# Optimization experiments

Hardware: AMD Instinct MI355X
Metric: run time of the kernel (lower is better)

The kernel has to match this reference:

```python
import jax, jax.numpy as jnp
import numpy as np

N_LEVELS = 12
BASE_RES = 16
PER_LEVEL_SCALE = 2.0
TABLE_SIZE = 1 << 20  # 2**log2_hashmap_size
PRIME_Y = np.uint32(2654435761)
FIRST_OMEGA = 300.0
HIDDEN_OMEGA = 1.0


def hash_grid_encode(table, coords):
    """tcnn-style multi-resolution hash grid, linear interpolation.
    table: [L, T, F] float32, coords: [N, 2] in [0, 1). Returns [N, L*F]."""
    feats = []
    for lvl in range(N_LEVELS):
        res = int(np.floor(BASE_RES * (PER_LEVEL_SCALE ** lvl)))
        pos = coords * res                       # [N, 2]
        i0 = jnp.floor(pos)
        w = pos - i0                             # fractional part, [N, 2]
        i0 = i0.astype(jnp.int32)
        dense = (res + 1) ** 2 <= TABLE_SIZE     # static per level
        acc = 0.0
        for dx, dy in ((0, 0), (1, 0), (0, 1), (1, 1)):
            ix = i0[:, 0] + dx
            iy = i0[:, 1] + dy
            if dense:
                idx = ix + iy * (res + 1)
            else:
                h = ix.astype(jnp.uint32) ^ (iy.astype(jnp.uint32) * PRIME_Y)
                idx = (h & jnp.uint32(TABLE_SIZE - 1)).astype(jnp.int32)
            wx = w[:, 0] if dx else (1.0 - w[:, 0])
            wy = w[:, 1] if dy else (1.0 - w[:, 1])
            acc = acc + table[lvl, idx] * (wx * wy)[:, None]
        feats.append(acc)
    return jnp.concatenate(feats, axis=-1)       # [N, 24]


def setup_inputs() -> dict:
    key = jax.random.key(0)
    ks = jax.random.split(key, 12)
    N = 1 << 20
    coords = jax.random.uniform(ks[0], (N, 2), dtype=jnp.float32)
    # tcnn default grid init: uniform(-1e-4, 1e-4)
    table = jax.random.uniform(ks[1], (N_LEVELS, TABLE_SIZE, 2), dtype=jnp.float32,
                               minval=-1e-4, maxval=1e-4)
    # first layer: normal(0, 0.1) per first_init_type='normal'
    W0 = 0.1 * jax.random.normal(ks[2], (24, 16), dtype=jnp.float32)
    b0 = jax.random.uniform(ks[3], (16,), dtype=jnp.float32,
                            minval=-1 / np.sqrt(24), maxval=1 / np.sqrt(24))
    # siren init for hidden/final: uniform(+-sqrt(6/fan_in)/omega), omega=1
    bnd = np.sqrt(6.0 / 16.0)
    W1 = jax.random.uniform(ks[4], (16, 16), jnp.float32, -bnd, bnd)
    b1 = jax.random.uniform(ks[5], (16,), jnp.float32, -0.25, 0.25)
    W2 = jax.random.uniform(ks[6], (16, 16), jnp.float32, -bnd, bnd)
    b2 = jax.random.uniform(ks[7], (16,), jnp.float32, -0.25, 0.25)
    W3 = jax.random.uniform(ks[8], (16, 1), jnp.float32, -bnd, bnd)
    b3 = jax.random.uniform(ks[9], (1,), jnp.float32, -0.25, 0.25)
    return {"coords": coords, "table": table, "W0": W0, "b0": b0,
            "W1": W1, "b1": b1, "W2": W2, "b2": b2, "W3": W3, "b3": b3}


def reference(coords, table, W0, b0, W1, b1, W2, b2, W3, b3):
    enc = hash_grid_encode(table, coords)               # [N, 24]
    h = jnp.sin(FIRST_OMEGA * (enc @ W0 + b0))          # SineLayer, omega_0=300
    h = jnp.sin(HIDDEN_OMEGA * (h @ W1 + b1))
    h = jnp.sin(HIDDEN_OMEGA * (h @ W2 + b2))
    return h @ W3 + b3                                  # outermost linear, [N, 1]
```

## Files before the change

### kernel.cpp

```cpp
#include <hip/hip_runtime.h>
#include <math.h>

#define TSIZE (1u << 20)
#define PRIME_Y 2654435761u
#define NHASH 6

typedef __attribute__((ext_vector_type(8))) short short8;
typedef __attribute__((ext_vector_type(4))) float f32x4;
typedef __attribute__((ext_vector_type(4))) float float4v;
typedef __attribute__((ext_vector_type(2))) float float2v;
typedef __attribute__((ext_vector_type(4))) unsigned uint4v;
typedef __attribute__((ext_vector_type(2))) unsigned uint2v;

struct alignas(8) f4a8 { float x, y, z, w; };

__device__ __forceinline__ unsigned bf16rne(unsigned u) {
    return (u + 0x7fffu + ((u >> 16) & 1u)) >> 16;
}
__device__ __forceinline__ unsigned pack_bf16x2(float a, float b) {
    return (bf16rne(__float_as_uint(a)) & 0xffffu) | (bf16rne(__float_as_uint(b)) << 16);
}
__device__ __forceinline__ float2 unpack_bf16x2(unsigned u) {
    float2 r;
    r.x = __uint_as_float(u << 16);
    r.y = __uint_as_float(u & 0xffff0000u);
    return r;
}
__device__ __forceinline__ short f2bf(float x) {
    return (short)(bf16rne(__float_as_uint(x)) & 0xffffu);
}
__device__ __forceinline__ float bf2f(short h) {
    return __uint_as_float(((unsigned)(unsigned short)h) << 16);
}
__device__ __forceinline__ unsigned hilo_pack(float v) {
    const unsigned uv = __float_as_uint(v);
    const float l = v - __uint_as_float(uv & 0xffff0000u);
    return (uv >> 16) | (__float_as_uint(l) & 0xffff0000u);
}

__device__ __forceinline__ unsigned fp8e(float f) {
    const float v = f * 8192.0f;
    const unsigned a = __float_as_uint(v);
    const unsigned sign = (a >> 31) << 7;
    const unsigned mag = a & 0x7fffffffu;
    const unsigned r = mag + 0x7ffffu + ((mag >> 20) & 1u);
    int u = (int)(r >> 20) - (120 << 3);
    u = (u < 0) ? 0 : u;
    return (unsigned)u | sign;
}
__device__ __forceinline__ float fp8d(unsigned u8) {
    const unsigned bits = ((u8 & 0x80u) << 24) |
                          (((u8 & 0x7fu) << 20) + (107u << 23));
    return __uint_as_float(bits);
}
__device__ __forceinline__ float2 fp8d2(unsigned u16) {
    float2 r;
    r.x = fp8d(u16 & 0xffu);
    r.y = fp8d((u16 >> 8) & 0xffu);
    return r;
}

__global__ __launch_bounds__(256) void convert_kernel(
    const float* __restrict__ table, unsigned* __restrict__ wtab8,
    const float* __restrict__ W0, const float* __restrict__ b0,
    const float* __restrict__ W1, const float* __restrict__ b1,
    const float* __restrict__ W2, const float* __restrict__ b2,
    const float* __restrict__ W3,
    uint4v* __restrict__ wfrag)
{
    if (blockIdx.x == 0 && threadIdx.x < 64) {
        const int lane = threadIdx.x;
        const int n = lane & 15;
        const int kb = lane >> 4;
        short8 bf0, b1a, b1b, b2a, b2b;
        #pragma unroll
        for (int j = 0; j < 8; ++j) {
            const int k = kb * 8 + j;
            bf0[j] = (k < 24) ? f2bf(W0[k * 16 + n]) : (short)0;
            const int i = k >> 1;
            const float w1 = W1[i * 16 + n];
            const float w2 = W2[i * 16 + n];
            const short w1h = f2bf(w1), w2h = f2bf(w2);
            b1a[j] = w1h;
            b2a[j] = w2h;
            b1b[j] = (k & 1) ? (short)0 : f2bf(w1 - bf2f(w1h));
            b2b[j] = (k & 1) ? (short)0 : f2bf(w2 - bf2f(w2h));
        }
        union { short8 s; uint4v u; } cv;
        cv.s = bf0; wfrag[0 * 64 + lane] = cv.u;
        cv.s = b1a; wfrag[1 * 64 + lane] = cv.u;
        cv.s = b1b; wfrag[2 * 64 + lane] = cv.u;
        cv.s = b2a; wfrag[3 * 64 + lane] = cv.u;
        cv.s = b2b; wfrag[4 * 64 + lane] = cv.u;
        float4v bb;
        bb.x = b0[n]; bb.y = b1[n]; bb.z = b2[n]; bb.w = W3[n];
        union { float4v f; uint4v u; } cf; cf.f = bb;
        wfrag[5 * 64 + lane] = cf.u;
    }
    const size_t total4 = (size_t)NHASH * TSIZE / 2;
    const float4v* __restrict__ src =
        reinterpret_cast<const float4v*>(table + (size_t)6 * TSIZE * 2);
    for (size_t i = (size_t)blockIdx.x * 256 + threadIdx.x; i < total4;
         i += (size_t)gridDim.x * 256) {
        float4v v = __builtin_nontemporal_load(&src[i]);
        wtab8[i] = fp8e(v.x) | (fp8e(v.y) << 8) | (fp8e(v.z) << 16) | (fp8e(v.w) << 24);
    }
}

__global__ __launch_bounds__(256) void pass_all_kernel(
    const float* __restrict__ coords,
    const unsigned* __restrict__ wtab8,
    unsigned* __restrict__ wenc,
    int bpl, int N)
{
    const int lvl = blockIdx.x / bpl;
    const int gid = (blockIdx.x - lvl * bpl) * 256 + threadIdx.x;
    const int base = gid * 4;
    if (base >= N) return;
    const int res = 16 << (lvl + 6);
    const unsigned* __restrict__ tlp = wtab8 + ((size_t)lvl * TSIZE >> 1);
    const unsigned short* __restrict__ tl8 =
        reinterpret_cast<const unsigned short*>(tlp);
    unsigned* __restrict__ we = wenc + (size_t)lvl * N;

    if (base + 3 < N) {
        const float4v* __restrict__ c4 = reinterpret_cast<const float4v*>(coords);
        const float4v ca = __builtin_nontemporal_load(&c4[gid * 2]);
        const float4v cb = __builtin_nontemporal_load(&c4[gid * 2 + 1]);
        const float xs[4] = {ca.x, ca.z, cb.x, cb.z};
        const float ys[4] = {ca.y, ca.w, cb.y, cb.w};
        unsigned h00a[4], h01a[4], h10a[4], h11a[4], oddp[4];
        float wxs[4], wys[4];
        #pragma unroll
        for (int p = 0; p < 4; ++p) {
            const float px = xs[p] * (float)res;
            const float py = ys[p] * (float)res;
            const float fx = floorf(px), fy = floorf(py);
            wxs[p] = px - fx;
            wys[p] = py - fy;
            const unsigned ux = (unsigned)(int)fx, uy = (unsigned)(int)fy;
            const unsigned hy0 = uy * PRIME_Y;
            const unsigned hy1 = (uy + 1u) * PRIME_Y;
            h00a[p] = (ux ^ hy0) & (TSIZE - 1u);
            h01a[p] = (ux ^ hy1) & (TSIZE - 1u);
            h10a[p] = ((ux + 1u) ^ hy0) & (TSIZE - 1u);
            h11a[p] = ((ux + 1u) ^ hy1) & (TSIZE - 1u);
            oddp[p] = ux & 1u;
        }
        unsigned pr0[4], pr1[4];
        #pragma unroll
        for (int p = 0; p < 4; ++p) {
            pr0[p] = tlp[h00a[p] >> 1];
            pr1[p] = tlp[h01a[p] >> 1];
        }
        unsigned t10[4], t11[4];
        #pragma unroll
        for (int p = 0; p < 4; ++p) { t10[p] = 0u; t11[p] = 0u; }
        #pragma unroll
        for (int p = 0; p < 4; ++p) {
            if (oddp[p]) {
                t10[p] = tl8[h10a[p]];
                t11[p] = tl8[h11a[p]];
            }
        }
        uint4v r;
        #pragma unroll
        for (int p = 0; p < 4; ++p) {
            const unsigned s0 = h00a[p] & 1u;
            const unsigned s1 = h01a[p] & 1u;
            const unsigned e00 = s0 ? (pr0[p] >> 16) : (pr0[p] & 0xffffu);
            const unsigned e01 = s1 ? (pr1[p] >> 16) : (pr1[p] & 0xffffu);
            const unsigned e10 = oddp[p] ? t10[p]
                                         : (s0 ? (pr0[p] & 0xffffu) : (pr0[p] >> 16));
            const unsigned e11 = oddp[p] ? t11[p]
                                         : (s1 ? (pr1[p] & 0xffffu) : (pr1[p] >> 16));
            const float wx = wxs[p], wy = wys[p];
            const float w00 = (1.0f - wx) * (1.0f - wy);
            const float w10 = wx * (1.0f - wy);
            const float w01 = (1.0f - wx) * wy;
            const float w11 = wx * wy;
            const float2 f00 = fp8d2(e00);
            const float2 f10 = fp8d2(e10);
            const float2 f01 = fp8d2(e01);
            const float2 f11 = fp8d2(e11);
            const float e0 = f00.x * w00 + f10.x * w10 + f01.x * w01 + f11.x * w11;
            const float e1 = f00.y * w00 + f10.y * w10 + f01.y * w01 + f11.y * w11;
            r[p] = pack_bf16x2(e0, e1);
        }
        ((uint4v*)we)[gid] = r;
    } else {
        for (int p = 0; p < 4 && base + p < N; ++p) {
            const float2 c = reinterpret_cast<const float2*>(coords)[base + p];
            const float px = c.x * (float)res;
            const float py = c.y * (float)res;
            const float fx = floorf(px), fy = floorf(py);
            const float wx = px - fx, wy = py - fy;
            const unsigned ux = (unsigned)(int)fx, uy = (unsigned)(int)fy;
            const unsigned hy0 = uy * PRIME_Y;
            const unsigned hy1 = (uy + 1u) * PRIME_Y;
            const float2 v00 = fp8d2(tl8[(ux ^ hy0) & (TSIZE - 1u)]);
            const float2 v10 = fp8d2(tl8[((ux + 1u) ^ hy0) & (TSIZE - 1u)]);
            const float2 v01 = fp8d2(tl8[(ux ^ hy1) & (TSIZE - 1u)]);
            const float2 v11 = fp8d2(tl8[((ux + 1u) ^ hy1) & (TSIZE - 1u)]);
            const float w00 = (1.0f - wx) * (1.0f - wy);
            const float w10 = wx * (1.0f - wy);
            const float w01 = (1.0f - wx) * wy;
            const float w11 = wx * wy;
            const float e0 = v00.x * w00 + v10.x * w10 + v01.x * w01 + v11.x * w11;
            const float e1 = v00.y * w00 + v10.y * w10 + v01.y * w01 + v11.y * w11;
            we[base + p] = pack_bf16x2(e0, e1);
        }
    }
}

__device__ __forceinline__ void stage_row(char* ldsw, int lane, const unsigned* u) {
    uint4v* rowp = (uint4v*)(ldsw + lane * 80);
    uint4v r0; r0.x = u[0]; r0.y = u[1]; r0.z = u[2]; r0.w = u[3];
    uint4v r1; r1.x = u[4]; r1.y = u[5]; r1.z = u[6]; r1.w = u[7];
    uint4v r2; r2.x = u[8]; r2.y = u[9]; r2.z = u[10]; r2.w = u[11];
    uint4v r3; r3.x = 0u; r3.y = 0u; r3.z = 0u; r3.w = 0u;
    rowp[0] = r0; rowp[1] = r1; rowp[2] = r2; rowp[3] = r3;
}

__global__ __launch_bounds__(256) void mlp_kernel(
    const float* __restrict__ coords,
    const float* __restrict__ table,
    const unsigned* __restrict__ wenc,
    const uint4v* __restrict__ wfrag,
    const float* __restrict__ b3p,
    float* __restrict__ out, int N)
{
    __shared__ char lds[40960];
    const int t = threadIdx.x;
    const int lane = t & 63;
    const int wv = t >> 6;
    const int n = lane & 15;
    const int kb = lane >> 4;
    char* lds0 = lds + wv * 10240;
    char* lds1 = lds0 + 5120;

    union { short8 s; uint4v u; } w0u, w1au, w1bu, w2au, w2bu;
    w0u.u  = wfrag[0 * 64 + lane];
    w1au.u = wfrag[1 * 64 + lane];
    w1bu.u = wfrag[2 * 64 + lane];
    w2au.u = wfrag[3 * 64 + lane];
    w2bu.u = wfrag[4 * 64 + lane];
    const short8 bf0 = w0u.s, b1a = w1au.s, b1b = w1bu.s, b2a = w2au.s, b2b = w2bu.s;
    union { float4v f; uint4v u; } cf;
    cf.u = wfrag[5 * 64 + lane];
    const float b0n = cf.f.x, b1n = cf.f.y, b2n = cf.f.z, w3n = cf.f.w;
    const float b3s = b3p[0];

    const int base = blockIdx.x * 512 + wv * 128;
    const int idx0 = base + lane;
    const int idx1 = idx0 + 64;
    const int i0 = (idx0 < N) ? idx0 : (N - 1);
    const int i1 = (idx1 < N) ? idx1 : (N - 1);

    unsigned u0[12], u1[12];
    #pragma unroll
    for (int l = 0; l < NHASH; ++l) {
        u0[6 + l] = wenc[(size_t)l * N + i0];
        u1[6 + l] = wenc[(size_t)l * N + i1];
    }
    const float2v cA = reinterpret_cast<const float2v*>(coords)[i0];
    const float2v cB = reinterpret_cast<const float2v*>(coords)[i1];

    #pragma unroll
    for (int lvl = 0; lvl < 6; ++lvl) {
        const int res = 16 << lvl;
        const int stride = res + 1;
        const float* __restrict__ tl = table + (size_t)lvl * TSIZE * 2u;
        {
            const float px = cA.x * (float)res;
            const float py = cA.y * (float)res;
            const float fx = floorf(px), fy = floorf(py);
            const float wx = px - fx, wy = py - fy;
            const int b = (int)fx + (int)fy * stride;
            const f4a8 r0 = *reinterpret_cast<const f4a8*>(tl + 2 * (size_t)b);
            const f4a8 r1 = *reinterpret_cast<const f4a8*>(tl + 2 * (size_t)(b + stride));
            const float w00 = (1.0f - wx) * (1.0f - wy);
            const float w10 = wx * (1.0f - wy);
            const float w01 = (1.0f - wx) * wy;
            const float w11 = wx * wy;
            u0[lvl] = pack_bf16x2(r0.x * w00 + r0.z * w10 + r1.x * w01 + r1.z * w11,
                                  r0.y * w00 + r0.w * w10 + r1.y * w01 + r1.w * w11);
        }
        {
            const float px = cB.x * (float)res;
            const float py = cB.y * (float)res;
            const float fx = floorf(px), fy = floorf(py);
            const float wx = px - fx, wy = py - fy;
            const int b = (int)fx + (int)fy * stride;
            const f4a8 r0 = *reinterpret_cast<const f4a8*>(tl + 2 * (size_t)b);
            const f4a8 r1 = *reinterpret_cast<const f4a8*>(tl + 2 * (size_t)(b + stride));
            const float w00 = (1.0f - wx) * (1.0f - wy);
            const float w10 = wx * (1.0f - wy);
            const float w01 = (1.0f - wx) * wy;
            const float w11 = wx * wy;
            u1[lvl] = pack_bf16x2(r0.x * w00 + r0.z * w10 + r1.x * w01 + r1.z * w11,
                                  r0.y * w00 + r0.w * w10 + r1.y * w01 + r1.w * w11);
        }
    }

    stage_row(lds0, lane, u0);
    stage_row(lds1, lane, u1);

    short8 a0[4], a1[4];
    #pragma unroll
    for (int m = 0; m < 4; ++m) {
        a0[m] = *(const short8*)(lds0 + (m * 16 + n) * 80 + kb * 16);
        a1[m] = *(const short8*)(lds1 + (m * 16 + n) * 80 + kb * 16);
    }

    const f32x4 z = {0.f, 0.f, 0.f, 0.f};
    f32x4 acc0[4], acc1[4];
    #pragma unroll
    for (int m = 0; m < 4; ++m) {
        acc0[m] = __builtin_amdgcn_mfma_f32_16x16x32_bf16(a0[m], bf0, z, 0, 0, 0);
        acc1[m] = __builtin_amdgcn_mfma_f32_16x16x32_bf16(a1[m], bf0, z, 0, 0, 0);
    }

    unsigned* hp0 = (unsigned*)lds0;
    unsigned* hp1 = (unsigned*)lds1;

    #pragma unroll
    for (int m = 0; m < 4; ++m) {
        #pragma unroll
        for (int r = 0; r < 4; ++r) {
            const int row = m * 16 + kb * 4 + r;
            hp0[row * 20 + n] = hilo_pack(__sinf(300.0f * (acc0[m][r] + b0n)));
            hp1[row * 20 + n] = hilo_pack(__sinf(300.0f * (acc1[m][r] + b0n)));
        }
    }
    #pragma unroll
    for (int m = 0; m < 4; ++m) {
        a0[m] = *(const short8*)(lds0 + (m * 16 + n) * 80 + kb * 16);
        a1[m] = *(const short8*)(lds1 + (m * 16 + n) * 80 + kb * 16);
    }
    #pragma unroll
    for (int m = 0; m < 4; ++m) {
        f32x4 p0 = __builtin_amdgcn_mfma_f32_16x16x32_bf16(a0[m], b1a, z, 0, 0, 0);
        acc0[m] = __builtin_amdgcn_mfma_f32_16x16x32_bf16(a0[m], b1b, p0, 0, 0, 0);
        f32x4 p1 = __builtin_amdgcn_mfma_f32_16x16x32_bf16(a1[m], b1a, z, 0, 0, 0);
        acc1[m] = __builtin_amdgcn_mfma_f32_16x16x32_bf16(a1[m], b1b, p1, 0, 0, 0);
    }

    #pragma unroll
    for (int m = 0; m < 4; ++m) {
        #pragma unroll
        for (int r = 0; r < 4; ++r) {
            const int row = m * 16 + kb * 4 + r;
            hp0[row * 20 + n] = hilo_pack(__sinf(acc0[m][r] + b1n));
            hp1[row * 20 + n] = hilo_pack(__sinf(acc1[m][r] + b1n));
        }
    }
    #pragma unroll
    for (int m = 0; m < 4; ++m) {
        a0[m] = *(const short8*)(lds0 + (m * 16 + n) * 80 + kb * 16);
        a1[m] = *(const short8*)(lds1 + (m * 16 + n) * 80 + kb * 16);
    }
    #pragma unroll
    for (int m = 0; m < 4; ++m) {
        f32x4 p0 = __builtin_amdgcn_mfma_f32_16x16x32_bf16(a0[m], b2a, z, 0, 0, 0);
        acc0[m] = __builtin_amdgcn_mfma_f32_16x16x32_bf16(a0[m], b2b, p0, 0, 0, 0);
        f32x4 p1 = __builtin_amdgcn_mfma_f32_16x16x32_bf16(a1[m], b2a, z, 0, 0, 0);
        acc1[m] = __builtin_amdgcn_mfma_f32_16x16x32_bf16(a1[m], b2b, p1, 0, 0, 0);
    }

    const int m2 = n >> 2, r2 = n & 3;
    float ov0 = 0.f, ov1 = 0.f;
    #pragma unroll
    for (int m = 0; m < 4; ++m) {
        #pragma unroll
        for (int r = 0; r < 4; ++r) {
            float v0 = __sinf(acc0[m][r] + b2n) * w3n;
            float v1 = __sinf(acc1[m][r] + b2n) * w3n;
            v0 += __shfl_xor(v0, 1);  v1 += __shfl_xor(v1, 1);
            v0 += __shfl_xor(v0, 2);  v1 += __shfl_xor(v1, 2);
            v0 += __shfl_xor(v0, 4);  v1 += __shfl_xor(v1, 4);
            v0 += __shfl_xor(v0, 8);  v1 += __shfl_xor(v1, 8);
            if (m == m2 && r == r2) { ov0 = v0; ov1 = v1; }
        }
    }
    const int g0 = base + m2 * 16 + kb * 4 + r2;
    const int g1 = g0 + 64;
    if (g0 < N) __builtin_nontemporal_store(ov0 + b3s, &out[g0]);
    if (g1 < N) __builtin_nontemporal_store(ov1 + b3s, &out[g1]);
}

__global__ __launch_bounds__(256) void hashsiren_fused(
    const float* __restrict__ coords,
    const float* __restrict__ table,
    const float* __restrict__ W0, const float* __restrict__ b0,
    const float* __restrict__ W1, const float* __restrict__ b1,
    const float* __restrict__ W2, const float* __restrict__ b2,
    const float* __restrict__ W3, const float* __restrict__ b3,
    float* __restrict__ out, int N)
{
    __shared__ float sW0[384];
    __shared__ float sW1[256];
    __shared__ float sW2[256];
    __shared__ float sb0[16], sb1[16], sb2[16], sW3[16];
    __shared__ float sb3;

    const int t = threadIdx.x;
    for (int i = t; i < 384; i += 256) sW0[i] = W0[i];
    sW1[t] = W1[t];
    sW2[t] = W2[t];
    if (t < 16) { sb0[t] = b0[t]; sb1[t] = b1[t]; sb2[t] = b2[t]; sW3[t] = W3[t]; }
    if (t == 0) sb3 = b3[0];
    __syncthreads();

    const int idx = blockIdx.x * 256 + t;
    if (idx >= N) return;

    const float2 c = reinterpret_cast<const float2*>(coords)[idx];

    float2 hv00[6], hv10[6], hv01[6], hv11[6];
    float hwx[6], hwy[6];
    #pragma unroll
    for (int l = 0; l < 6; ++l) {
        const int res = 16 << (l + 6);
        const float px = c.x * (float)res;
        const float py = c.y * (float)res;
        const float fx = floorf(px), fy = floorf(py);
        hwx[l] = px - fx;
        hwy[l] = py - fy;
        const unsigned ux = (unsigned)(int)fx, uy = (unsigned)(int)fy;
        const unsigned hy0 = uy * PRIME_Y;
        const unsigned hy1 = (uy + 1u) * PRIME_Y;
        const float2* __restrict__ tl =
            reinterpret_cast<const float2*>(table) + (size_t)(l + 6) * TSIZE;
        hv00[l] = tl[(ux ^ hy0) & (TSIZE - 1u)];
        hv10[l] = tl[((ux + 1u) ^ hy0) & (TSIZE - 1u)];
        hv01[l] = tl[(ux ^ hy1) & (TSIZE - 1u)];
        hv11[l] = tl[((ux + 1u) ^ hy1) & (TSIZE - 1u)];
    }

    float enc[24];
    #pragma unroll
    for (int lvl = 0; lvl < 6; ++lvl) {
        const int res = 16 << lvl;
        const float px = c.x * (float)res;
        const float py = c.y * (float)res;
        const float fx = floorf(px), fy = floorf(py);
        const float wx = px - fx, wy = py - fy;
        const int ix = (int)fx, iy = (int)fy;
        const int stride = res + 1;
        const int base = ix + iy * stride;
        const float2* __restrict__ tl =
            reinterpret_cast<const float2*>(table) + (size_t)lvl * TSIZE;
        const float2 v00 = tl[base];
        const float2 v10 = tl[base + 1];
        const float2 v01 = tl[base + stride];
        const float2 v11 = tl[base + stride + 1];
        const float w00 = (1.0f - wx) * (1.0f - wy);
        const float w10 = wx * (1.0f - wy);
        const float w01 = (1.0f - wx) * wy;
        const float w11 = wx * wy;
        enc[2 * lvl]     = v00.x * w00 + v10.x * w10 + v01.x * w01 + v11.x * w11;
        enc[2 * lvl + 1] = v00.y * w00 + v10.y * w10 + v01.y * w01 + v11.y * w11;
    }
    #pragma unroll
    for (int l = 0; l < 6; ++l) {
        const float wx = hwx[l], wy = hwy[l];
        const float w00 = (1.0f - wx) * (1.0f - wy);
        const float w10 = wx * (1.0f - wy);
        const float w01 = (1.0f - wx) * wy;
        const float w11 = wx * wy;
        enc[2 * (l + 6)]     = hv00[l].x * w00 + hv10[l].x * w10 + hv01[l].x * w01 + hv11[l].x * w11;
        enc[2 * (l + 6) + 1] = hv00[l].y * w00 + hv10[l].y * w10 + hv01[l].y * w01 + hv11[l].y * w11;
    }

    float h0[16];
    #pragma unroll
    for (int j = 0; j < 16; ++j) {
        float aa = sb0[j];
        #pragma unroll
        for (int k = 0; k < 24; ++k) aa += enc[k] * sW0[k * 16 + j];
        h0[j] = __sinf(300.0f * aa);
    }
    float h1[16];
    #pragma unroll
    for (int j = 0; j < 16; ++j) {
        float aa = sb1[j];
        #pragma unroll
        for (int k = 0; k < 16; ++k) aa += h0[k] * sW1[k * 16 + j];
        h1[j] = __sinf(aa);
    }
    float h2[16];
    #pragma unroll
    for (int j = 0; j < 16; ++j) {
        float aa = sb2[j];
        #pragma unroll
        for (int k = 0; k < 16; ++k) aa += h1[k] * sW2[k * 16 + j];
        h2[j] = __sinf(aa);
    }
    float o = sb3;
    #pragma unroll
    for (int k = 0; k < 16; ++k) o += h2[k] * sW3[k];
    out[idx] = o;
}

extern "C" void kernel_launch(void* const* d_in, const int* in_sizes, int n_in,
                              void* d_out, int out_size, void* d_ws, size_t ws_size,
                              hipStream_t stream) {
    const float* coords = (const float*)d_in[0];
    const float* table  = (const float*)d_in[1];
    const float* W0 = (const float*)d_in[2];
    const float* b0 = (const float*)d_in[3];
    const float* W1 = (const float*)d_in[4];
    const float* b1 = (const float*)d_in[5];
    const float* W2 = (const float*)d_in[6];
    const float* b2 = (const float*)d_in[7];
    const float* W3 = (const float*)d_in[8];
    const float* b3 = (const float*)d_in[9];
    float* out = (float*)d_out;

    const int N = in_sizes[0] / 2;

    const size_t tab_w = (size_t)NHASH * TSIZE / 2;
    const size_t enc_w = (size_t)NHASH * (size_t)N;
    const size_t need = tab_w * 4 + enc_w * 4 + 6144;
    if (ws_size >= need) {
        unsigned* wtab8 = (unsigned*)d_ws;
        unsigned* wenc = wtab8 + tab_w;
        uint4v* wfrag = (uint4v*)(wenc + enc_w);
        convert_kernel<<<4096, 256, 0, stream>>>(table, wtab8,
                                                 W0, b0, W1, b1, W2, b2, W3, wfrag);
        const int bpl = (N + 1023) / 1024;
        pass_all_kernel<<<NHASH * bpl, 256, 0, stream>>>(coords, wtab8, wenc, bpl, N);
        mlp_kernel<<<(N + 511) / 512, 256, 0, stream>>>(coords, table, wenc, wfrag,
                                                        b3, out, N);
    } else {
        const int block = 256;
        const int grid = (N + block - 1) / block;
        hashsiren_fused<<<grid, block, 0, stream>>>(coords, table,
                                                    W0, b0, W1, b1, W2, b2, W3, b3,
                                                    out, N);
    }
}
```

Baseline: 148.7 us.

## Pack dense grid levels into bf16 paired-cell table and vectorize per-point I/O

Adds a conversion pass that stores the six dense grid levels as bf16 with each cell paired with its x+1 neighbor, so the MLP kernel fetches two 8-byte loads per corner pair instead of fp32 16-byte loads. Each lane now handles two adjacent points, so wenc, coords and outputs are read and written with wider vector accesses. This shrinks the dense-level gather footprint and improves cache hit rate, at the cost of extra conversion work and bf16 precision on dense levels.

```diff
diff --git a/kernel.cpp b/kernel.cpp
--- a/kernel.cpp
+++ b/kernel.cpp
@@ -4,6 +4,8 @@
 #define TSIZE (1u << 20)
 #define PRIME_Y 2654435761u
 #define NHASH 6
+#define NDENSE_CELLS 351462
+#define NDENSE_PAD   351488
 
 typedef __attribute__((ext_vector_type(8))) short short8;
 typedef __attribute__((ext_vector_type(4))) float f32x4;
@@ -11,8 +13,6 @@
 typedef __attribute__((ext_vector_type(2))) float float2v;
 typedef __attribute__((ext_vector_type(4))) unsigned uint4v;
 typedef __attribute__((ext_vector_type(2))) unsigned uint2v;
-
-struct alignas(8) f4a8 { float x, y, z, w; };
 
 __device__ __forceinline__ unsigned bf16rne(unsigned u) {
     return (u + 0x7fffu + ((u >> 16) & 1u)) >> 16;
@@ -62,6 +62,7 @@
 
 __global__ __launch_bounds__(256) void convert_kernel(
     const float* __restrict__ table, unsigned* __restrict__ wtab8,
+    unsigned* __restrict__ wdense,
     const float* __restrict__ W0, const float* __restrict__ b0,
     const float* __restrict__ W1, const float* __restrict__ b1,
     const float* __restrict__ W2, const float* __restrict__ b2,
@@ -104,6 +105,21 @@
          i += (size_t)gridDim.x * 256) {
         float4v v = __builtin_nontemporal_load(&src[i]);
         wtab8[i] = fp8e(v.x) | (fp8e(v.y) << 8) | (fp8e(v.z) << 16) | (fp8e(v.w) << 24);
+    }
+    const int DCUM[7] = {0, 289, 1378, 5603, 22244, 88293, 351462};
+    for (int i = blockIdx.x * 256 + threadIdx.x; i < NDENSE_CELLS;
+         i += gridDim.x * 256) {
+        int lvl = 0;
+        #pragma unroll
+        for (int l = 1; l < 6; ++l) lvl += (i >= DCUM[l]);
+        const int e = i - DCUM[lvl];
+        const int sz = DCUM[lvl + 1] - DCUM[lvl];
+        const float* __restrict__ dsrc = table + (size_t)lvl * TSIZE * 2u;
+        const int e1 = (e + 1 < sz) ? e + 1 : e;
+        uint2v o;
+        o.x = pack_bf16x2(dsrc[2 * e], dsrc[2 * e + 1]);
+        o.y = pack_bf16x2(dsrc[2 * e1], dsrc[2 * e1 + 1]);
+        reinterpret_cast<uint2v*>(wdense)[i] = o;
     }
 }
 
@@ -224,7 +240,7 @@
 
 __global__ __launch_bounds__(256) void mlp_kernel(
     const float* __restrict__ coords,
-    const float* __restrict__ table,
+    const unsigned* __restrict__ wdense,
     const unsigned* __restrict__ wenc,
     const uint4v* __restrict__ wfrag,
     const float* __restrict__ b3p,
@@ -251,40 +267,46 @@
     const float b0n = cf.f.x, b1n = cf.f.y, b2n = cf.f.z, w3n = cf.f.w;
     const float b3s = b3p[0];
 
-    const int base = blockIdx.x * 512 + wv * 128;
-    const int idx0 = base + lane;
-    const int idx1 = idx0 + 64;
-    const int i0 = (idx0 < N) ? idx0 : (N - 1);
-    const int i1 = (idx1 < N) ? idx1 : (N - 1);
+    const int wbase = blockIdx.x * 512 + wv * 128;
+    int i0 = wbase + 2 * lane;
+    if (i0 > N - 2) i0 = (N - 2) & ~1;
 
     unsigned u0[12], u1[12];
     #pragma unroll
     for (int l = 0; l < NHASH; ++l) {
-        u0[6 + l] = wenc[(size_t)l * N + i0];
-        u1[6 + l] = wenc[(size_t)l * N + i1];
-    }
-    const float2v cA = reinterpret_cast<const float2v*>(coords)[i0];
-    const float2v cB = reinterpret_cast<const float2v*>(coords)[i1];
-
+        const uint2v ev = *reinterpret_cast<const uint2v*>(wenc + (size_t)l * N + i0);
+        u0[6 + l] = ev.x;
+        u1[6 + l] = ev.y;
+    }
+    const float4v cc = reinterpret_cast<const float4v*>(coords)[i0 >> 1];
+    const float2 cA = {cc.x, cc.y};
+    const float2 cB = {cc.z, cc.w};
+
+    const int DC[6] = {0, 289, 1378, 5603, 22244, 88293};
     #pragma unroll
     for (int lvl = 0; lvl < 6; ++lvl) {
         const int res = 16 << lvl;
         const int stride = res + 1;
-        const float* __restrict__ tl = table + (size_t)lvl * TSIZE * 2u;
+        const uint2v* __restrict__ td =
+            reinterpret_cast<const uint2v*>(wdense) + DC[lvl];
         {
             const float px = cA.x * (float)res;
             const float py = cA.y * (float)res;
             const float fx = floorf(px), fy = floorf(py);
             const float wx = px - fx, wy = py - fy;
             const int b = (int)fx + (int)fy * stride;
-            const f4a8 r0 = *reinterpret_cast<const f4a8*>(tl + 2 * (size_t)b);
-            const f4a8 r1 = *reinterpret_cast<const f4a8*>(tl + 2 * (size_t)(b + stride));
+            const uint2v r0 = td[b];
+            const uint2v r1 = td[b + stride];
+            const float2 v00 = unpack_bf16x2(r0.x);
+            const float2 v10 = unpack_bf16x2(r0.y);
+            const float2 v01 = unpack_bf16x2(r1.x);
+            const float2 v11 = unpack_bf16x2(r1.y);
             const float w00 = (1.0f - wx) * (1.0f - wy);
             const float w10 = wx * (1.0f - wy);
             const float w01 = (1.0f - wx) * wy;
             const float w11 = wx * wy;
-            u0[lvl] = pack_bf16x2(r0.x * w00 + r0.z * w10 + r1.x * w01 + r1.z * w11,
-                                  r0.y * w00 + r0.w * w10 + r1.y * w01 + r1.w * w11);
+            u0[lvl] = pack_bf16x2(v00.x * w00 + v10.x * w10 + v01.x * w01 + v11.x * w11,
+                                  v00.y * w00 + v10.y * w10 + v01.y * w01 + v11.y * w11);
         }
         {
             const float px = cB.x * (float)res;
@@ -292,14 +314,18 @@
             const float fx = floorf(px), fy = floorf(py);
             const float wx = px - fx, wy = py - fy;
             const int b = (int)fx + (int)fy * stride;
-            const f4a8 r0 = *reinterpret_cast<const f4a8*>(tl + 2 * (size_t)b);
-            const f4a8 r1 = *reinterpret_cast<const f4a8*>(tl + 2 * (size_t)(b + stride));
+            const uint2v r0 = td[b];
+            const uint2v r1 = td[b + stride];
+            const float2 v00 = unpack_bf16x2(r0.x);
+            const float2 v10 = unpack_bf16x2(r0.y);
+            const float2 v01 = unpack_bf16x2(r1.x);
+            const float2 v11 = unpack_bf16x2(r1.y);
             const float w00 = (1.0f - wx) * (1.0f - wy);
             const float w10 = wx * (1.0f - wy);
             const float w01 = (1.0f - wx) * wy;
             const float w11 = wx * wy;
-            u1[lvl] = pack_bf16x2(r0.x * w00 + r0.z * w10 + r1.x * w01 + r1.z * w11,
-                                  r0.y * w00 + r0.w * w10 + r1.y * w01 + r1.w * w11);
+            u1[lvl] = pack_bf16x2(v00.x * w00 + v10.x * w10 + v01.x * w01 + v11.x * w11,
+                                  v00.y * w00 + v10.y * w10 + v01.y * w01 + v11.y * w11);
         }
     }
 
@@ -383,10 +409,14 @@
             if (m == m2 && r == r2) { ov0 = v0; ov1 = v1; }
         }
     }
-    const int g0 = base + m2 * 16 + kb * 4 + r2;
-    const int g1 = g0 + 64;
-    if (g0 < N) __builtin_nontemporal_store(ov0 + b3s, &out[g0]);
-    if (g1 < N) __builtin_nontemporal_store(ov1 + b3s, &out[g1]);
+    const int row0 = m2 * 16 + kb * 4 + r2;
+    const int g0 = wbase + 2 * row0;
+    if (g0 + 1 < N) {
+        float2v o; o.x = ov0 + b3s; o.y = ov1 + b3s;
+        __builtin_nontemporal_store(o, reinterpret_cast<float2v*>(out + g0));
+    } else if (g0 < N) {
+        out[g0] = ov0 + b3s;
+    }
 }
 
 __global__ __launch_bounds__(256) void hashsiren_fused(
@@ -522,16 +552,18 @@
 
     const size_t tab_w = (size_t)NHASH * TSIZE / 2;
     const size_t enc_w = (size_t)NHASH * (size_t)N;
-    const size_t need = tab_w * 4 + enc_w * 4 + 6144;
-    if (ws_size >= need) {
+    const size_t dns_w = (size_t)NDENSE_PAD;
+    const size_t need = (tab_w + enc_w + dns_w * 2) * 4 + 6144;
+    if (ws_size >= need && N >= 2) {
         unsigned* wtab8 = (unsigned*)d_ws;
         unsigned* wenc = wtab8 + tab_w;
-        uint4v* wfrag = (uint4v*)(wenc + enc_w);
-        convert_kernel<<<4096, 256, 0, stream>>>(table, wtab8,
+        unsigned* wdense = wenc + enc_w;
+        uint4v* wfrag = (uint4v*)(wdense + dns_w * 2);
+        convert_kernel<<<4096, 256, 0, stream>>>(table, wtab8, wdense,
                                                  W0, b0, W1, b1, W2, b2, W3, wfrag);
         const int bpl = (N + 1023) / 1024;
         pass_all_kernel<<<NHASH * bpl, 256, 0, stream>>>(coords, wtab8, wenc, bpl, N);
-        mlp_kernel<<<(N + 511) / 512, 256, 0, stream>>>(coords, table, wenc, wfrag,
+        mlp_kernel<<<(N + 511) / 512, 256, 0, stream>>>(coords, wdense, wenc, wfrag,
                                                         b3, out, N);
     } else {
         const int block = 256;
```

Result: no change. 148.3 us (-0.2%).
